# Performance work log

Hardware: AMD Instinct MI355X
Metric: run time of the kernel (lower is better)

The kernel has to match this reference:

```python
import jax, jax.numpy as jnp
import numpy as np


def _cdist_p2(x, y):
    # x: [N, t1, h], y: [N, t2, h] -> [N, t1, t2] Euclidean distances
    x2 = jnp.sum(x * x, axis=-1)  # [N, t1]
    y2 = jnp.sum(y * y, axis=-1)  # [N, t2]
    xy = jnp.einsum('nik,njk->nij', x, y)  # [N, t1, t2]
    d2 = x2[:, :, None] + y2[None if False else slice(None), None, :] - 2.0 * xy
    d2 = jnp.maximum(d2, 0.0)
    return jnp.sqrt(d2)


def _solve_relaxed_wmd(scores, axis):
    # argmin + one-hot scatter + (mask*scores).mean() == sum of per-slice minima / scores.size
    idx = jnp.argmin(scores, axis=axis, keepdims=True)
    mins = jnp.take_along_axis(scores, idx, axis=axis)
    return jnp.sum(mins) / scores.size


def setup_inputs() -> dict:
    key = jax.random.key(0)
    kx, ky = jax.random.split(key)
    L, B, t1, t2, h = 4, 16, 1024, 1024, 128
    x = jax.random.normal(kx, (L, B, t1, h), dtype=jnp.float32)
    y = jax.random.normal(ky, (L, B, t2, h), dtype=jnp.float32)
    return {"x": x, "y": y}


def reference(x, y):
    L, B, t1, h = x.shape
    t2 = y.shape[2]
    xf = x.reshape(L * B, t1, h).astype(jnp.float32)
    yf = y.reshape(L * B, t2, h).astype(jnp.float32)
    scores = _cdist_p2(xf, yf)  # [L*B, t1, t2]
    forward_scores = _solve_relaxed_wmd(scores, axis=1)
    backward_scores = _solve_relaxed_wmd(scores, axis=2)
    return jnp.maximum(forward_scores, backward_scores)
```

## Files before the change

kernel.cpp:

```cpp
#include <hip/hip_runtime.h>

#define NB 64
#define T 1024
#define HD 128

#define EINF 0xFF800000u

typedef __attribute__((ext_vector_type(8))) short bf16x8;
typedef __attribute__((ext_vector_type(4))) float f32x4;

static __device__ __forceinline__ short f2bf(float f) {
    unsigned u = __float_as_uint(f);
    u += 0x7FFFu + ((u >> 16) & 1u);
    return (short)(u >> 16);
}
static __device__ __forceinline__ unsigned fenc(float f) {
    unsigned b = __float_as_uint(f);
    return b ^ (unsigned)(((int)b >> 31) | (int)0x80000000);
}
static __device__ __forceinline__ float fdec(unsigned u) {
    unsigned m = (~(unsigned)((int)u >> 31)) | 0x80000000u;
    return __uint_as_float(u ^ m);
}

__global__ void wmd_prep(const float* __restrict__ x, const float* __restrict__ y,
                         short* __restrict__ xbf, short* __restrict__ ybf,
                         float* __restrict__ x2, float* __restrict__ y2,
                         unsigned* __restrict__ g_colmin, unsigned* __restrict__ g_rowmin,
                         float* __restrict__ sums, unsigned* __restrict__ counter) {
    int gi = blockIdx.x * 256 + threadIdx.x;
    float4 vx = reinterpret_cast<const float4*>(x)[gi];
    float4 vy = reinterpret_cast<const float4*>(y)[gi];
    short4 sx, sy;
    sx.x = f2bf(vx.x); sx.y = f2bf(vx.y); sx.z = f2bf(vx.z); sx.w = f2bf(vx.w);
    sy.x = f2bf(vy.x); sy.y = f2bf(vy.y); sy.z = f2bf(vy.z); sy.w = f2bf(vy.w);
    reinterpret_cast<short4*>(xbf)[gi] = sx;
    reinterpret_cast<short4*>(ybf)[gi] = sy;
    float px = vx.x * vx.x + vx.y * vx.y + vx.z * vx.z + vx.w * vx.w;
    float py = vy.x * vy.x + vy.y * vy.y + vy.z * vy.z + vy.w * vy.w;
    px += __shfl_xor(px, 1);  px += __shfl_xor(px, 2);  px += __shfl_xor(px, 4);
    px += __shfl_xor(px, 8);  px += __shfl_xor(px, 16);
    py += __shfl_xor(py, 1);  py += __shfl_xor(py, 2);  py += __shfl_xor(py, 4);
    py += __shfl_xor(py, 8);  py += __shfl_xor(py, 16);
    if ((threadIdx.x & 31) == 0) { x2[gi >> 5] = px; y2[gi >> 5] = py; }
    if (gi < NB * T) { g_colmin[gi] = EINF; g_rowmin[gi] = EINF; }
    if (gi < 2) sums[gi] = 0.f;
    if (gi == 2) counter[0] = 0u;
}

__global__ __launch_bounds__(256, 4)
void wmd_main(const short* __restrict__ xbf, const short* __restrict__ ybf,
              const float* __restrict__ x2g, const float* __restrict__ y2g,
              unsigned* __restrict__ g_colmin, unsigned* __restrict__ g_rowmin) {
    __shared__ short b_sm[2][64 * 128];
    __shared__ float y2_sm[512];
    __shared__ unsigned col_min_sm[512];

    const int tid  = threadIdx.x;
    const int lin  = blockIdx.y * 16 + blockIdx.x;
    const int m    = (lin >> 3) & 7;
    const int grp  = ((lin >> 6) << 3) | (lin & 7);
    const int n    = grp >> 1;
    const int i0   = m * 128;
    const int j0   = (grp & 1) * 512;
    const int lane = tid & 63;
    const int wave = tid >> 6;
    const int l16  = lane & 15, quad = lane >> 4;
    const float FINF = __uint_as_float(0x7F800000u);

    #pragma unroll
    for (int e = tid; e < 512; e += 256) col_min_sm[e] = EINF;

#define ISSUE_GLLS(pbuf, jtile)                                                   \
    {                                                                             \
        const short* ybase = ybf + (((size_t)(n * T + j0 + (jtile) * 64)) << 7);  \
        _Pragma("unroll")                                                         \
        for (int it = 0; it < 4; ++it) {                                          \
            int g   = wave * 4 + it;                                              \
            int s   = g * 64 + lane;                                              \
            int row = s >> 4;                                                     \
            int c   = (s & 15) ^ (row & 7);                                       \
            const short* gp = ybase + row * 128 + c * 8;                          \
            __builtin_amdgcn_global_load_lds(                                     \
                (const __attribute__((address_space(1))) void*)gp,                \
                (__attribute__((address_space(3))) void*)&b_sm[pbuf][g * 512],    \
                16, 0, 0);                                                        \
        }                                                                         \
    }

    ISSUE_GLLS(0, 0);

    bf16x8 af[2][4];
    #pragma unroll
    for (int mi = 0; mi < 2; ++mi)
        #pragma unroll
        for (int kk = 0; kk < 4; ++kk)
            af[mi][kk] = *reinterpret_cast<const bf16x8*>(
                xbf + (((size_t)(n * T + i0 + wave * 32 + mi * 16 + l16)) << 7)
                    + kk * 32 + quad * 8);
    float x2v[8];
    #pragma unroll
    for (int mi = 0; mi < 2; ++mi)
        #pragma unroll
        for (int r = 0; r < 4; ++r)
            x2v[mi * 4 + r] = x2g[n * T + i0 + wave * 32 + mi * 16 + quad * 4 + r];
    #pragma unroll
    for (int e = tid; e < 512; e += 256) y2_sm[e] = y2g[n * T + j0 + e];

    float rmin[8];
    #pragma unroll
    for (int q = 0; q < 8; ++q) rmin[q] = FINF;

    __syncthreads();

    for (int jt = 0; jt < 8; ++jt) {
        const int p = jt & 1;
        if (jt < 7) ISSUE_GLLS(p ^ 1, jt + 1);

        float y2v[4];
        #pragma unroll
        for (int ni = 0; ni < 4; ++ni)
            y2v[ni] = y2_sm[jt * 64 + ni * 16 + l16];

        f32x4 acc[2][4];
        #pragma unroll
        for (int mi = 0; mi < 2; ++mi)
            #pragma unroll
            for (int ni = 0; ni < 4; ++ni) {
                f32x4 z = {0.f, 0.f, 0.f, 0.f};
                acc[mi][ni] = z;
            }

        #pragma unroll
        for (int kk = 0; kk < 4; ++kk) {
            bf16x8 bv[4];
            #pragma unroll
            for (int ni = 0; ni < 4; ++ni) {
                int row = ni * 16 + l16;
                int c   = (kk * 4 + quad) ^ (row & 7);
                bv[ni] = *reinterpret_cast<const bf16x8*>(&b_sm[p][(row * 16 + c) * 8]);
            }
            #pragma unroll
            for (int mi = 0; mi < 2; ++mi)
                #pragma unroll
                for (int ni = 0; ni < 4; ++ni)
                    acc[mi][ni] = __builtin_amdgcn_mfma_f32_16x16x32_bf16(
                        af[mi][kk], bv[ni], acc[mi][ni], 0, 0, 0);
        }

        float vcol[4] = {FINF, FINF, FINF, FINF};
        #pragma unroll
        for (int mi = 0; mi < 2; ++mi)
            #pragma unroll
            for (int r = 0; r < 4; ++r) {
                float x2r = x2v[mi * 4 + r];
                #pragma unroll
                for (int ni = 0; ni < 4; ++ni) {
                    float xy = acc[mi][ni][r];
                    rmin[mi * 4 + r] = fminf(rmin[mi * 4 + r], fmaf(-2.f, xy, y2v[ni]));
                    vcol[ni]         = fminf(vcol[ni],         fmaf(-2.f, xy, x2r));
                }
            }
        #pragma unroll
        for (int ni = 0; ni < 4; ++ni) {
            float v = vcol[ni];
            v = fminf(v, __shfl_xor(v, 16));
            v = fminf(v, __shfl_xor(v, 32));
            if (lane < 16)
                atomicMin(&col_min_sm[jt * 64 + ni * 16 + lane], fenc(v));
        }
        __syncthreads();
    }

    #pragma unroll
    for (int mi = 0; mi < 2; ++mi)
        #pragma unroll
        for (int r = 0; r < 4; ++r) {
            float v = rmin[mi * 4 + r];
            v = fminf(v, __shfl_xor(v, 1));
            v = fminf(v, __shfl_xor(v, 2));
            v = fminf(v, __shfl_xor(v, 4));
            v = fminf(v, __shfl_xor(v, 8));
            if (l16 == 0)
                atomicMin(&g_rowmin[n * T + i0 + wave * 32 + mi * 16 + quad * 4 + r], fenc(v));
        }
    #pragma unroll
    for (int e = tid; e < 512; e += 256)
        atomicMin(&g_colmin[n * T + j0 + e], col_min_sm[e]);
}

__global__ void wmd_reduce(const unsigned* __restrict__ g_colmin,
                           const unsigned* __restrict__ g_rowmin,
                           const float* __restrict__ x2g,
                           const float* __restrict__ y2g,
                           float* __restrict__ sums,
                           unsigned* __restrict__ counter,
                           float* __restrict__ out) {
    int n = blockIdx.x, t = threadIdx.x;
    float sc = 0.f, sr = 0.f;
    for (int e = t; e < T; e += 256) {
        float cv = fdec(g_colmin[n * T + e]) + y2g[n * T + e];
        float rv = fdec(g_rowmin[n * T + e]) + x2g[n * T + e];
        sc += sqrtf(fmaxf(cv, 0.f));
        sr += sqrtf(fmaxf(rv, 0.f));
    }
    #pragma unroll
    for (int o = 1; o < 64; o <<= 1) {
        sc += __shfl_xor(sc, o);
        sr += __shfl_xor(sr, o);
    }
    __shared__ float bc[4], br[4];
    int lane = t & 63, wv = t >> 6;
    if (lane == 0) { bc[wv] = sc; br[wv] = sr; }
    __syncthreads();
    if (t == 0) {
        atomicAdd(&sums[0], bc[0] + bc[1] + bc[2] + bc[3]);
        atomicAdd(&sums[1], br[0] + br[1] + br[2] + br[3]);
        __threadfence();
        unsigned old = atomicAdd(counter, 1u);
        if (old == NB - 1) {
            float a = atomicAdd(&sums[0], 0.f);
            float b = atomicAdd(&sums[1], 0.f);
            out[0] = fmaxf(a, b) * (1.0f / 67108864.0f);
        }
    }
}

extern "C" void kernel_launch(void* const* d_in, const int* in_sizes, int n_in,
                              void* d_out, int out_size, void* d_ws, size_t ws_size,
                              hipStream_t stream) {
    const float* x = (const float*)d_in[0];
    const float* y = (const float*)d_in[1];
    float* out = (float*)d_out;

    char* ws = (char*)d_ws;
    unsigned* g_colmin = (unsigned*)(ws);
    unsigned* g_rowmin = (unsigned*)(ws + 256 * 1024);
    float*    x2g      = (float*)(ws + 512 * 1024);
    float*    y2g      = (float*)(ws + 768 * 1024);
    float*    sums     = (float*)(ws + 1024 * 1024);
    unsigned* counter  = (unsigned*)(ws + 1024 * 1024 + 8);
    short*    xbf      = (short*)(ws + 2 * 1024 * 1024);
    short*    ybf      = (short*)(ws + 20 * 1024 * 1024);

    wmd_prep<<<(NB * T * HD / 4) / 256, 256, 0, stream>>>(
        x, y, xbf, ybf, x2g, y2g, g_colmin, g_rowmin, sums, counter);
    wmd_main<<<dim3(16, NB), 256, 0, stream>>>(xbf, ybf, x2g, y2g, g_colmin, g_rowmin);
    wmd_reduce<<<NB, 256, 0, stream>>>(g_colmin, g_rowmin, x2g, y2g, sums, counter, out);
}
```

Baseline: 127.7 us.

## Convert x to bf16 inside main kernel and fuse final reduction via last-block counters

The prep kernel no longer writes a bf16 copy of x. The main kernel instead loads fp32 x directly and converts its A-fragments in registers. The separate reduce kernel is removed: each block increments a per-batch counter, and the last of the 16 blocks for a batch computes that batch's sqrt sums, with a global counter finalizing the output. This cuts a 32MB write and read of xbf plus one kernel launch, at the cost of doubled x load bytes in the main kernel and extra fences and atomics.

```diff
diff --git a/kernel.cpp b/kernel.cpp
--- a/kernel.cpp
+++ b/kernel.cpp
@@ -24,17 +24,16 @@
 }
 
 __global__ void wmd_prep(const float* __restrict__ x, const float* __restrict__ y,
-                         short* __restrict__ xbf, short* __restrict__ ybf,
+                         short* __restrict__ ybf,
                          float* __restrict__ x2, float* __restrict__ y2,
                          unsigned* __restrict__ g_colmin, unsigned* __restrict__ g_rowmin,
-                         float* __restrict__ sums, unsigned* __restrict__ counter) {
+                         float* __restrict__ sums, unsigned* __restrict__ batch_cnt,
+                         unsigned* __restrict__ g_cnt) {
     int gi = blockIdx.x * 256 + threadIdx.x;
     float4 vx = reinterpret_cast<const float4*>(x)[gi];
     float4 vy = reinterpret_cast<const float4*>(y)[gi];
-    short4 sx, sy;
-    sx.x = f2bf(vx.x); sx.y = f2bf(vx.y); sx.z = f2bf(vx.z); sx.w = f2bf(vx.w);
+    short4 sy;
     sy.x = f2bf(vy.x); sy.y = f2bf(vy.y); sy.z = f2bf(vy.z); sy.w = f2bf(vy.w);
-    reinterpret_cast<short4*>(xbf)[gi] = sx;
     reinterpret_cast<short4*>(ybf)[gi] = sy;
     float px = vx.x * vx.x + vx.y * vx.y + vx.z * vx.z + vx.w * vx.w;
     float py = vy.x * vy.x + vy.y * vy.y + vy.z * vy.z + vy.w * vy.w;
@@ -45,16 +44,21 @@
     if ((threadIdx.x & 31) == 0) { x2[gi >> 5] = px; y2[gi >> 5] = py; }
     if (gi < NB * T) { g_colmin[gi] = EINF; g_rowmin[gi] = EINF; }
     if (gi < 2) sums[gi] = 0.f;
-    if (gi == 2) counter[0] = 0u;
+    if (gi < NB + 66 && gi >= 2) batch_cnt[gi - 2] = 0u;
+    if (gi == NB + 66) g_cnt[0] = 0u;
 }
 
 __global__ __launch_bounds__(256, 4)
-void wmd_main(const short* __restrict__ xbf, const short* __restrict__ ybf,
+void wmd_main(const float* __restrict__ x, const short* __restrict__ ybf,
               const float* __restrict__ x2g, const float* __restrict__ y2g,
-              unsigned* __restrict__ g_colmin, unsigned* __restrict__ g_rowmin) {
+              unsigned* __restrict__ g_colmin, unsigned* __restrict__ g_rowmin,
+              float* __restrict__ sums, unsigned* __restrict__ batch_cnt,
+              unsigned* __restrict__ g_cnt, float* __restrict__ out) {
     __shared__ short b_sm[2][64 * 128];
     __shared__ float y2_sm[512];
     __shared__ unsigned col_min_sm[512];
+    __shared__ unsigned last_sm;
+    __shared__ float red_sm[8];
 
     const int tid  = threadIdx.x;
     const int lin  = blockIdx.y * 16 + blockIdx.x;
@@ -94,10 +98,15 @@
     #pragma unroll
     for (int mi = 0; mi < 2; ++mi)
         #pragma unroll
-        for (int kk = 0; kk < 4; ++kk)
-            af[mi][kk] = *reinterpret_cast<const bf16x8*>(
-                xbf + (((size_t)(n * T + i0 + wave * 32 + mi * 16 + l16)) << 7)
-                    + kk * 32 + quad * 8);
+        for (int kk = 0; kk < 4; ++kk) {
+            const float4* gp = reinterpret_cast<const float4*>(
+                x + (((size_t)(n * T + i0 + wave * 32 + mi * 16 + l16)) << 7) + kk * 32 + quad * 8);
+            float4 a = gp[0], b = gp[1];
+            bf16x8 f;
+            f[0] = f2bf(a.x); f[1] = f2bf(a.y); f[2] = f2bf(a.z); f[3] = f2bf(a.w);
+            f[4] = f2bf(b.x); f[5] = f2bf(b.y); f[6] = f2bf(b.z); f[7] = f2bf(b.w);
+            af[mi][kk] = f;
+        }
     float x2v[8];
     #pragma unroll
     for (int mi = 0; mi < 2; ++mi)
@@ -187,40 +196,37 @@
     #pragma unroll
     for (int e = tid; e < 512; e += 256)
         atomicMin(&g_colmin[n * T + j0 + e], col_min_sm[e]);
-}
-
-__global__ void wmd_reduce(const unsigned* __restrict__ g_colmin,
-                           const unsigned* __restrict__ g_rowmin,
-                           const float* __restrict__ x2g,
-                           const float* __restrict__ y2g,
-                           float* __restrict__ sums,
-                           unsigned* __restrict__ counter,
-                           float* __restrict__ out) {
-    int n = blockIdx.x, t = threadIdx.x;
+
+    __threadfence();
+    if (tid == 0) last_sm = atomicAdd(&batch_cnt[n], 1u);
+    __syncthreads();
+    if (last_sm != 15u) return;
+
+    __threadfence();
     float sc = 0.f, sr = 0.f;
-    for (int e = t; e < T; e += 256) {
-        float cv = fdec(g_colmin[n * T + e]) + y2g[n * T + e];
-        float rv = fdec(g_rowmin[n * T + e]) + x2g[n * T + e];
-        sc += sqrtf(fmaxf(cv, 0.f));
-        sr += sqrtf(fmaxf(rv, 0.f));
+    for (int e = tid; e < T; e += 256) {
+        unsigned cu = __hip_atomic_load(&g_colmin[n * T + e], __ATOMIC_RELAXED,
+                                        __HIP_MEMORY_SCOPE_AGENT);
+        unsigned ru = __hip_atomic_load(&g_rowmin[n * T + e], __ATOMIC_RELAXED,
+                                        __HIP_MEMORY_SCOPE_AGENT);
+        sc += sqrtf(fmaxf(fdec(cu) + y2g[n * T + e], 0.f));
+        sr += sqrtf(fmaxf(fdec(ru) + x2g[n * T + e], 0.f));
     }
     #pragma unroll
     for (int o = 1; o < 64; o <<= 1) {
         sc += __shfl_xor(sc, o);
         sr += __shfl_xor(sr, o);
     }
-    __shared__ float bc[4], br[4];
-    int lane = t & 63, wv = t >> 6;
-    if (lane == 0) { bc[wv] = sc; br[wv] = sr; }
+    if (lane == 0) { red_sm[wave] = sc; red_sm[4 + wave] = sr; }
     __syncthreads();
-    if (t == 0) {
-        atomicAdd(&sums[0], bc[0] + bc[1] + bc[2] + bc[3]);
-        atomicAdd(&sums[1], br[0] + br[1] + br[2] + br[3]);
+    if (tid == 0) {
+        atomicAdd(&sums[0], red_sm[0] + red_sm[1] + red_sm[2] + red_sm[3]);
+        atomicAdd(&sums[1], red_sm[4] + red_sm[5] + red_sm[6] + red_sm[7]);
         __threadfence();
-        unsigned old = atomicAdd(counter, 1u);
+        unsigned old = atomicAdd(g_cnt, 1u);
         if (old == NB - 1) {
-            float a = atomicAdd(&sums[0], 0.f);
-            float b = atomicAdd(&sums[1], 0.f);
+            float a = __hip_atomic_load(&sums[0], __ATOMIC_RELAXED, __HIP_MEMORY_SCOPE_AGENT);
+            float b = __hip_atomic_load(&sums[1], __ATOMIC_RELAXED, __HIP_MEMORY_SCOPE_AGENT);
             out[0] = fmaxf(a, b) * (1.0f / 67108864.0f);
         }
     }
@@ -234,17 +240,17 @@
     float* out = (float*)d_out;
 
     char* ws = (char*)d_ws;
-    unsigned* g_colmin = (unsigned*)(ws);
-    unsigned* g_rowmin = (unsigned*)(ws + 256 * 1024);
-    float*    x2g      = (float*)(ws + 512 * 1024);
-    float*    y2g      = (float*)(ws + 768 * 1024);
-    float*    sums     = (float*)(ws + 1024 * 1024);
-    unsigned* counter  = (unsigned*)(ws + 1024 * 1024 + 8);
-    short*    xbf      = (short*)(ws + 2 * 1024 * 1024);
-    short*    ybf      = (short*)(ws + 20 * 1024 * 1024);
+    unsigned* g_colmin  = (unsigned*)(ws);
+    unsigned* g_rowmin  = (unsigned*)(ws + 256 * 1024);
+    float*    x2g       = (float*)(ws + 512 * 1024);
+    float*    y2g       = (float*)(ws + 768 * 1024);
+    float*    sums      = (float*)(ws + 1024 * 1024);
+    unsigned* batch_cnt = (unsigned*)(ws + 1024 * 1024 + 256);
+    unsigned* g_cnt     = (unsigned*)(ws + 1024 * 1024 + 2048);
+    short*    ybf       = (short*)(ws + 2 * 1024 * 1024);
 
     wmd_prep<<<(NB * T * HD / 4) / 256, 256, 0, stream>>>(
-        x, y, xbf, ybf, x2g, y2g, g_colmin, g_rowmin, sums, counter);
-    wmd_main<<<dim3(16, NB), 256, 0, stream>>>(xbf, ybf, x2g, y2g, g_colmin, g_rowmin);
-    wmd_reduce<<<NB, 256, 0, stream>>>(g_colmin, g_rowmin, x2g, y2g, sums, counter, out);
-}
+        x, y, ybf, x2g, y2g, g_colmin, g_rowmin, sums, batch_cnt, g_cnt);
+    wmd_main<<<dim3(16, NB), 256, 0, stream>>>(
+        x, ybf, x2g, y2g, g_colmin, g_rowmin, sums, batch_cnt, g_cnt, out);
+}
```

Measured after the change: 194.9 us. 1.53x slower.
